# Performance work log

Measured on AMD Instinct MI355X. Metric: run time of the kernel, lower is better.

Reference implementation:

```python
import jax, jax.numpy as jnp
import numpy as np

EMBED_DIM = 1024
NUM_HEADS = 16
HEAD_DIM = EMBED_DIM // NUM_HEADS
VOCAB = 5          # languages
BOTTLENECK = 800
SCALING = HEAD_DIM ** -0.5


def setup_inputs() -> dict:
    key = jax.random.key(0)
    ks = jax.random.split(key, 16)
    T, B, D = 2048, 2, EMBED_DIM
    s = 0.02
    return {
        "query": jax.random.normal(ks[0], (T, B, D), jnp.float32),
        "key": jax.random.normal(ks[1], (T, B, D), jnp.float32),
        "value": jax.random.normal(ks[2], (T, B, D), jnp.float32),
        "wq": jax.random.normal(ks[3], (D, D), jnp.float32) * s,
        "bq": jnp.zeros((D,), jnp.float32),
        "wk": jax.random.normal(ks[4], (D, D), jnp.float32) * s,
        "bk": jnp.zeros((D,), jnp.float32),
        "wv": jax.random.normal(ks[5], (D, D), jnp.float32) * s,
        "bv": jnp.zeros((D,), jnp.float32),
        "wo": jax.random.normal(ks[6], (D, D), jnp.float32) * s,
        "bo": jnp.zeros((D,), jnp.float32),
        "wte": jax.random.normal(ks[7], (VOCAB, D), jnp.float32) * s,
        "ct_w1": jax.random.normal(ks[8], (VOCAB, BOTTLENECK, D), jnp.float32) * s,
        "ct_b1": jnp.zeros((VOCAB, BOTTLENECK), jnp.float32),
        "ct_w2": jax.random.normal(ks[9], (VOCAB, 2 * D, BOTTLENECK), jnp.float32) * s,
        "ct_b2": jnp.zeros((VOCAB, 2 * D), jnp.float32),
        "language_id": jax.random.randint(ks[10], (B,), 0, VOCAB, jnp.int32),
    }


def _prefix_kv(language_id, wte, ct_w1, ct_b1, ct_w2, ct_b2):
    # PrefixTuningLangEmbLangspec: embed lang id, run all 5 bottleneck MLPs,
    # select per-sample MLP output via one-hot weighting, split into K/V.
    B = language_id.shape[0]
    emb = wte[language_id]                                  # [B, D]
    h = jnp.tanh(jnp.einsum("bd,chd->cbh", emb, ct_w1) + ct_b1[:, None, :])  # [5,B,800]
    kv = jnp.einsum("cbh,cdh->cbd", h, ct_w2) + ct_b2[:, None, :]            # [5,B,2D]
    w = jax.nn.one_hot(language_id, VOCAB, dtype=kv.dtype)  # [B,5]
    kv_sel = jnp.einsum("bc,cbd->bd", w, kv)                # [B,2D]
    # view(b,1,2,nh,hd): first D -> keys, second D -> values
    pk = kv_sel[:, :EMBED_DIM].reshape(B, NUM_HEADS, 1, HEAD_DIM)
    pv = kv_sel[:, EMBED_DIM:].reshape(B, NUM_HEADS, 1, HEAD_DIM)
    return pk, pv


def reference(query, key, value, wq, bq, wk, bk, wv, bv, wo, bo,
              wte, ct_w1, ct_b1, ct_w2, ct_b2, language_id):
    T, B, D = query.shape
    pk, pv = _prefix_kv(language_id, wte, ct_w1, ct_b1, ct_w2, ct_b2)  # [B,H,1,hd]

    # separate Q/K/V projections (Linear: x @ W^T + b)
    q = (jnp.einsum("tbd,ed->tbe", query, wq) + bq) * SCALING
    k = jnp.einsum("tbd,ed->tbe", key, wk) + bk
    v = jnp.einsum("tbd,ed->tbe", value, wv) + bv

    # [T,B,D] -> [B,H,T,hd]
    def split_heads(x):
        return x.reshape(T, B, NUM_HEADS, HEAD_DIM).transpose(1, 2, 0, 3)

    qh = split_heads(q)
    kh = jnp.concatenate([pk, split_heads(k)], axis=2)  # [B,H,T+1,hd]
    vh = jnp.concatenate([pv, split_heads(v)], axis=2)

    scores = jnp.einsum("bhqd,bhkd->bhqk", qh, kh)      # [B,H,T,T+1]
    attn = jax.nn.softmax(scores, axis=-1)
    ctx = jnp.einsum("bhqk,bhkd->bhqd", attn, vh)       # [B,H,T,hd]

    ctx = ctx.transpose(2, 0, 1, 3).reshape(T, B, D)    # back to [T,B,D]
    out = jnp.einsum("tbd,ed->tbe", ctx, wo) + bo
    return out
```

## Files before the change

### kernel.cpp

```cpp
#include <hip/hip_runtime.h>
#include <stdint.h>

#define T_SEQ 2048
#define BATCH 2
#define DIM   1024
#define NH    16
#define HD    64
#define TKP   2112

typedef _Float16 v8h __attribute__((ext_vector_type(8)));
typedef _Float16 v4h __attribute__((ext_vector_type(4)));
typedef float    f32x4 __attribute__((ext_vector_type(4)));

__device__ __forceinline__ void gload16(const _Float16* g, _Float16* l) {
  __builtin_amdgcn_global_load_lds(
      (__attribute__((address_space(1))) unsigned int*)g,
      (__attribute__((address_space(3))) unsigned int*)l, 16, 0, 0);
}

__global__ void cvt_all(const float4* __restrict__ s0, const float4* __restrict__ s1,
                        const float4* __restrict__ s2, const float4* __restrict__ s3,
                        const float4* __restrict__ s4, const float4* __restrict__ s5,
                        const float4* __restrict__ s6,
                        v4h* __restrict__ d0, v4h* __restrict__ d1, v4h* __restrict__ d2,
                        v4h* __restrict__ d3, v4h* __restrict__ d4, v4h* __restrict__ d5,
                        v4h* __restrict__ d6) {
  const int NTB4 = 1048576, DD4 = 262144;
  int i = blockIdx.x * 256 + threadIdx.x;
  const float4* s; v4h* d; int off;
  if (i < 3 * NTB4) {
    int t = i / NTB4; off = i - t * NTB4;
    s = t == 0 ? s0 : t == 1 ? s1 : s2;
    d = t == 0 ? d0 : t == 1 ? d1 : d2;
  } else {
    int j = i - 3 * NTB4;
    int t = j / DD4; off = j - t * DD4;
    s = t == 0 ? s3 : t == 1 ? s4 : t == 2 ? s5 : s6;
    d = t == 0 ? d3 : t == 1 ? d4 : t == 2 ? d5 : d6;
  }
  float4 v = s[off];
  v4h o = { (_Float16)v.x, (_Float16)v.y, (_Float16)v.z, (_Float16)v.w };
  d[off] = o;
}

__global__ void prefix_h_k(const float* __restrict__ wte, const float* __restrict__ w1,
                           const float* __restrict__ b1, const int* __restrict__ lang,
                           float* __restrict__ hbuf) {
  int wid = blockIdx.x * 4 + (threadIdx.x >> 6);
  int lane = threadIdx.x & 63;
  int b = wid / 800, j = wid - b * 800;
  int c = lang[b];
  const float* wr = w1 + ((size_t)c * 800 + j) * 1024;
  const float* em = wte + (size_t)c * 1024;
  float s = 0.f;
  for (int d = lane; d < 1024; d += 64) s += wr[d] * em[d];
  for (int off = 32; off > 0; off >>= 1) s += __shfl_down(s, off, 64);
  if (lane == 0) hbuf[wid] = tanhf(s + b1[c * 800 + j]);
}

__global__ void prefix_kv_k(const float* __restrict__ w2, const float* __restrict__ b2,
                            const float* __restrict__ hbuf, const int* __restrict__ lang,
                            _Float16* __restrict__ kb, _Float16* __restrict__ vb) {
  int wid = blockIdx.x * 4 + (threadIdx.x >> 6);
  int lane = threadIdx.x & 63;
  int b = wid >> 11, e = wid & 2047;
  int c = lang[b];
  const float* wr = w2 + ((size_t)c * 2048 + e) * 800;
  const float* hb = hbuf + b * 800;
  float s = 0.f;
  for (int j = lane; j < 800; j += 64) s += wr[j] * hb[j];
  for (int off = 32; off > 0; off >>= 1) s += __shfl_down(s, off, 64);
  if (lane == 0) {
    float val = s + b2[c * 2048 + e];
    if (e < 1024) {
      int h = e >> 6, hd = e & 63;
      kb[((size_t)(b * 16 + h) * TKP + 2048) * 64 + hd] = (_Float16)val;
    } else {
      int d = e - 1024;
      int h = d >> 6, hd = d & 63;
      vb[((size_t)(b * 16 + h) * 64 + hd) * TKP + 2048] = (_Float16)val;
    }
  }
}

__global__ void pad_k(_Float16* kb, _Float16* vb) {
  int bh = blockIdx.x;
  v8h z = {};
  _Float16* kp = kb + ((size_t)bh * TKP + 2048) * 64;
  for (int i = threadIdx.x; i < 512; i += 256) *(v8h*)&kp[i * 8] = z;
  for (int i = threadIdx.x; i < 512; i += 256) {
    int c = i >> 3, seg = i & 7;
    *(v8h*)&vb[((size_t)bh * 64 + c) * TKP + 2048 + seg * 8] = z;
  }
}

__global__ __launch_bounds__(256) void gemm_bt_k(
    const _Float16* __restrict__ A0, const _Float16* __restrict__ A1, const _Float16* __restrict__ A2,
    const _Float16* __restrict__ W0, const _Float16* __restrict__ W1, const _Float16* __restrict__ W2,
    const float* __restrict__ bs0, const float* __restrict__ bs1, const float* __restrict__ bs2,
    _Float16* __restrict__ qb, _Float16* __restrict__ kb, _Float16* __restrict__ vb,
    float* __restrict__ fout, int mode_base)
{
  __shared__ __align__(16) _Float16 smem[128 * 64 * 2];
  _Float16* As = smem;
  _Float16* Bs = smem + 128 * 64;
  const int mode = mode_base + blockIdx.z;
  const _Float16* A = (mode == 1) ? A1 : (mode == 2) ? A2 : A0;
  const _Float16* W = (mode == 1) ? W1 : (mode == 2) ? W2 : W0;
  const float* bias = (mode == 1) ? bs1 : (mode == 2) ? bs2 : bs0;
  const int tid = threadIdx.x, w = tid >> 6, lane = tid & 63;
  const int quad = lane >> 4, l15 = lane & 15;
  const int r0 = blockIdx.x * 128, c0 = blockIdx.y * 128;
  const int wm = w >> 1, wn = w & 1;
  const int srow = lane >> 3, sseg = lane & 7;
  f32x4 acc[4][4] = {};
  for (int k0 = 0; k0 < 1024; k0 += 64) {
    for (int i = 0; i < 4; ++i) {
      int rowb = w * 32 + i * 8;
      gload16(A + (size_t)(r0 + rowb + srow) * 1024 + k0 + sseg * 8, &As[rowb * 64]);
      gload16(W + (size_t)(c0 + rowb + srow) * 1024 + k0 + sseg * 8, &Bs[rowb * 64]);
    }
    __syncthreads();
    for (int ks = 0; ks < 2; ++ks) {
      v8h af[4], bfr[4];
      for (int mt = 0; mt < 4; ++mt)
        af[mt] = *(const v8h*)&As[(wm * 64 + mt * 16 + l15) * 64 + ks * 32 + quad * 8];
      for (int nt = 0; nt < 4; ++nt)
        bfr[nt] = *(const v8h*)&Bs[(wn * 64 + nt * 16 + l15) * 64 + ks * 32 + quad * 8];
      for (int mt = 0; mt < 4; ++mt)
        for (int nt = 0; nt < 4; ++nt)
          acc[mt][nt] = __builtin_amdgcn_mfma_f32_16x16x32_f16(af[mt], bfr[nt], acc[mt][nt], 0, 0, 0);
    }
    __syncthreads();
  }
  if (mode == 3) {
    for (int nt = 0; nt < 4; ++nt) {
      int e = c0 + wn * 64 + nt * 16 + l15;
      float be = bias[e];
      for (int mt = 0; mt < 4; ++mt) {
        int rb = r0 + wm * 64 + mt * 16 + quad * 4;
        for (int reg = 0; reg < 4; ++reg)
          fout[(size_t)(rb + reg) * 1024 + e] = acc[mt][nt][reg] + be;
      }
    }
    return;
  }
  _Float16* st = smem + w * 4096;
  const float qscale = (mode == 0) ? 0.125f : 1.0f;
  for (int p = 0; p < 2; ++p) {
    __syncthreads();
    for (int ntl = 0; ntl < 2; ++ntl) {
      int nt = p * 2 + ntl;
      int e = c0 + wn * 64 + nt * 16 + l15;
      float be = bias[e];
      for (int mt = 0; mt < 4; ++mt)
        for (int reg = 0; reg < 4; ++reg) {
          float val = (acc[mt][nt][reg] + be) * qscale;
          int rl = mt * 16 + quad * 4 + reg;
          if (mode != 2) st[rl * 40 + ntl * 16 + l15] = (_Float16)val;
          else st[(ntl * 16 + l15) * 72 + (rl & 1) * 32 + (rl >> 1)] = (_Float16)val;
        }
    }
    __syncthreads();
    if (mode != 2) {
      for (int it = 0; it < 4; ++it) {
        int chunk = it * 64 + lane;
        int rr = chunk >> 2, seg = chunk & 3;
        v8h val = *(const v8h*)&st[rr * 40 + seg * 8];
        int r = r0 + wm * 64 + rr, b = r & 1, t = r >> 1;
        int e0 = c0 + wn * 64 + p * 32 + seg * 8;
        int h = e0 >> 6, hd0 = e0 & 63;
        if (mode == 0) *(v8h*)&qb[((size_t)(b * 16 + h) * 2048 + t) * 64 + hd0] = val;
        else           *(v8h*)&kb[((size_t)(b * 16 + h) * TKP + t) * 64 + hd0] = val;
      }
    } else {
      for (int it = 0; it < 4; ++it) {
        int chunk = it * 64 + lane;
        int el = chunk >> 3, b = (chunk >> 2) & 1, qs = chunk & 3;
        v8h val = *(const v8h*)&st[el * 72 + b * 32 + qs * 8];
        int e = c0 + wn * 64 + p * 32 + el;
        int h = e >> 6, hd = e & 63;
        int t0 = ((r0 + wm * 64) >> 1) + qs * 8;
        *(v8h*)&vb[((size_t)(b * 16 + h) * 64 + hd) * TKP + t0] = val;
      }
    }
  }
}

__global__ __launch_bounds__(256) void attn_k(
    const _Float16* __restrict__ qb, const _Float16* __restrict__ kb,
    const _Float16* __restrict__ vb, _Float16* __restrict__ ctx)
{
  __shared__ __align__(16) _Float16 Qs[128 * 72];
  __shared__ __align__(16) _Float16 Ks[64 * 72];
  __shared__ __align__(16) _Float16 Vs[64 * 72];
  __shared__ __align__(16) _Float16 Ps[128 * 72];
  const int bh = blockIdx.x;
  const int qt0 = blockIdx.y * 128;
  const int tid = threadIdx.x, w = tid >> 6, lane = tid & 63;
  const int quad = lane >> 4, l15 = lane & 15;
  for (int it = 0; it < 4; ++it) {
    int slot = it * 256 + tid;
    int row = slot >> 3, seg = slot & 7;
    int4 v = *(const int4*)(qb + ((size_t)bh * 2048 + qt0 + row) * 64 + seg * 8);
    *(int4*)&Qs[row * 72 + seg * 8] = v;
  }
  const int sr = tid >> 3, sseg = tid & 7;
  const _Float16* kptr = kb + (size_t)bh * TKP * 64 + sr * 64 + sseg * 8;
  const _Float16* vptr = vb + (size_t)bh * 64 * TKP + (size_t)sr * TKP + sseg * 8;
  int4 kp0 = *(const int4*)kptr, kp1 = *(const int4*)(kptr + 2048);
  int4 vp0 = *(const int4*)vptr, vp1 = *(const int4*)(vptr + 32 * TKP);
  kptr += 4096; vptr += 64;
  f32x4 O[4][2] = {};
  float l_[2] = { 0.f, 0.f };
  for (int kc = 0; kc < 33; ++kc) {
    __syncthreads();
    *(int4*)&Ks[sr * 72 + sseg * 8] = kp0;
    *(int4*)&Ks[(sr + 32) * 72 + sseg * 8] = kp1;
    *(int4*)&Vs[sr * 72 + sseg * 8] = vp0;
    *(int4*)&Vs[(sr + 32) * 72 + sseg * 8] = vp1;
    __syncthreads();
    if (kc < 32) {
      kp0 = *(const int4*)kptr; kp1 = *(const int4*)(kptr + 2048);
      vp0 = *(const int4*)vptr; vp1 = *(const int4*)(vptr + 32 * TKP);
      kptr += 4096; vptr += 64;
    }
    f32x4 S[4][2] = {};
    for (int ks = 0; ks < 2; ++ks) {
      v8h q0 = *(const v8h*)&Qs[(w * 32 + l15) * 72 + ks * 32 + quad * 8];
      v8h q1 = *(const v8h*)&Qs[(w * 32 + 16 + l15) * 72 + ks * 32 + quad * 8];
      for (int mt = 0; mt < 4; ++mt) {
        v8h ak = *(const v8h*)&Ks[(mt * 16 + l15) * 72 + ks * 32 + quad * 8];
        S[mt][0] = __builtin_amdgcn_mfma_f32_16x16x32_f16(ak, q0, S[mt][0], 0, 0, 0);
        S[mt][1] = __builtin_amdgcn_mfma_f32_16x16x32_f16(ak, q1, S[mt][1], 0, 0, 0);
      }
    }
    if (kc == 32) {
      for (int mt = 0; mt < 4; ++mt)
        for (int reg = 0; reg < 4; ++reg)
          if (mt * 16 + quad * 4 + reg > 0) { S[mt][0][reg] = -1e30f; S[mt][1][reg] = -1e30f; }
    }
    for (int nt = 0; nt < 2; ++nt) {
      float rsum = 0.f;
      for (int mt = 0; mt < 4; ++mt) {
        float p0 = __expf(S[mt][nt][0]);
        float p1 = __expf(S[mt][nt][1]);
        float p2 = __expf(S[mt][nt][2]);
        float p3 = __expf(S[mt][nt][3]);
        rsum += (p0 + p1) + (p2 + p3);
        v4h pk4 = { (_Float16)p0, (_Float16)p1, (_Float16)p2, (_Float16)p3 };
        *(v4h*)&Ps[(w * 32 + nt * 16 + l15) * 72 + mt * 16 + quad * 4] = pk4;
      }
      l_[nt] += rsum;
    }
    for (int ks = 0; ks < 2; ++ks) {
      v8h p0 = *(const v8h*)&Ps[(w * 32 + l15) * 72 + ks * 32 + quad * 8];
      v8h p1 = *(const v8h*)&Ps[(w * 32 + 16 + l15) * 72 + ks * 32 + quad * 8];
      for (int ht = 0; ht < 4; ++ht) {
        v8h av = *(const v8h*)&Vs[(ht * 16 + l15) * 72 + ks * 32 + quad * 8];
        O[ht][0] = __builtin_amdgcn_mfma_f32_16x16x32_f16(av, p0, O[ht][0], 0, 0, 0);
        O[ht][1] = __builtin_amdgcn_mfma_f32_16x16x32_f16(av, p1, O[ht][1], 0, 0, 0);
      }
    }
  }
  for (int nt = 0; nt < 2; ++nt) {
    l_[nt] += __shfl_xor(l_[nt], 16, 64);
    l_[nt] += __shfl_xor(l_[nt], 32, 64);
  }
  const int b = bh >> 4, hh = bh & 15;
  for (int nt = 0; nt < 2; ++nt) {
    float inv = 1.f / l_[nt];
    int q = qt0 + w * 32 + nt * 16 + l15;
    for (int ht = 0; ht < 4; ++ht) {
      v4h o4 = { (_Float16)(O[ht][nt][0] * inv), (_Float16)(O[ht][nt][1] * inv),
                 (_Float16)(O[ht][nt][2] * inv), (_Float16)(O[ht][nt][3] * inv) };
      *(v4h*)(ctx + ((size_t)q * 2 + b) * 1024 + hh * 64 + ht * 16 + quad * 4) = o4;
    }
  }
}

extern "C" void kernel_launch(void* const* d_in, const int* in_sizes, int n_in,
                              void* d_out, int out_size, void* d_ws, size_t ws_size,
                              hipStream_t stream) {
  (void)in_sizes; (void)n_in; (void)out_size; (void)ws_size;
  const float* query = (const float*)d_in[0];
  const float* key_  = (const float*)d_in[1];
  const float* value = (const float*)d_in[2];
  const float* wq = (const float*)d_in[3];
  const float* bq = (const float*)d_in[4];
  const float* wk = (const float*)d_in[5];
  const float* bk = (const float*)d_in[6];
  const float* wv = (const float*)d_in[7];
  const float* bv = (const float*)d_in[8];
  const float* wo = (const float*)d_in[9];
  const float* bo = (const float*)d_in[10];
  const float* wte = (const float*)d_in[11];
  const float* w1 = (const float*)d_in[12];
  const float* b1 = (const float*)d_in[13];
  const float* w2 = (const float*)d_in[14];
  const float* b2 = (const float*)d_in[15];
  const int* lang = (const int*)d_in[16];
  float* out = (float*)d_out;

  const size_t NTB = (size_t)T_SEQ * BATCH * DIM;
  const size_t DD  = (size_t)DIM * DIM;
  const size_t KVN = (size_t)BATCH * NH * TKP * HD;
  _Float16* xq  = (_Float16*)d_ws;
  _Float16* xk  = xq + NTB;
  _Float16* xv  = xk + NTB;
  _Float16* wqb = xv + NTB;
  _Float16* wkb = wqb + DD;
  _Float16* wvb = wkb + DD;
  _Float16* wob = wvb + DD;
  _Float16* qbuf = wob + DD;
  _Float16* kbuf = qbuf + NTB;
  _Float16* vbuf = kbuf + KVN;
  float* hbuf = (float*)(vbuf + KVN);
  _Float16* ctxb = xq;

  cvt_all<<<16384, 256, 0, stream>>>((const float4*)query, (const float4*)key_,
                                     (const float4*)value, (const float4*)wq,
                                     (const float4*)wk, (const float4*)wv, (const float4*)wo,
                                     (v4h*)xq, (v4h*)xk, (v4h*)xv, (v4h*)wqb,
                                     (v4h*)wkb, (v4h*)wvb, (v4h*)wob);
  pad_k<<<32, 256, 0, stream>>>(kbuf, vbuf);
  prefix_h_k<<<400, 256, 0, stream>>>(wte, w1, b1, lang, hbuf);
  prefix_kv_k<<<1024, 256, 0, stream>>>(w2, b2, hbuf, lang, kbuf, vbuf);
  gemm_bt_k<<<dim3(32, 8, 3), 256, 0, stream>>>(xq, xk, xv, wqb, wkb, wvb, bq, bk, bv,
                                                qbuf, kbuf, vbuf, nullptr, 0);
  attn_k<<<dim3(32, 16), 256, 0, stream>>>(qbuf, kbuf, vbuf, ctxb);
  gemm_bt_k<<<dim3(32, 8, 1), 256, 0, stream>>>(ctxb, ctxb, ctxb, wob, wob, wob, bo, bo, bo,
                                                qbuf, kbuf, vbuf, out, 3);
}
```

Before: 311.0 us.

## Double-buffer K/V in LDS, keep Q in registers, use exp2 and MFMA row sums

The attention kernel now double-buffers the K/V shared tiles, which removes one barrier per iteration. Q fragments are loaded straight into registers instead of being staged through LDS. The softmax scale is folded with log2(e) into the Q projection so the kernel can use the hardware exp2. Row sums are accumulated by an MFMA against a ones vector rather than scalar adds and cross-lane shuffles. This cuts LDS traffic, barrier cost and VALU work, in exchange for more LDS space for the doubled buffers and extra MFMA issue, with the row sum now taken over fp16-rounded probabilities.

```diff
diff --git a/kernel.cpp b/kernel.cpp
--- a/kernel.cpp
+++ b/kernel.cpp
@@ -146,7 +146,7 @@
     return;
   }
   _Float16* st = smem + w * 4096;
-  const float qscale = (mode == 0) ? 0.125f : 1.0f;
+  const float qscale = (mode == 0) ? 0.125f * 1.44269504088896341f : 1.0f;
   for (int p = 0; p < 2; ++p) {
     __syncthreads();
     for (int ntl = 0; ntl < 2; ++ntl) {
@@ -191,20 +191,18 @@
     const _Float16* __restrict__ qb, const _Float16* __restrict__ kb,
     const _Float16* __restrict__ vb, _Float16* __restrict__ ctx)
 {
-  __shared__ __align__(16) _Float16 Qs[128 * 72];
-  __shared__ __align__(16) _Float16 Ks[64 * 72];
-  __shared__ __align__(16) _Float16 Vs[64 * 72];
+  __shared__ __align__(16) _Float16 Ks[2][64 * 72];
+  __shared__ __align__(16) _Float16 Vs[2][64 * 72];
   __shared__ __align__(16) _Float16 Ps[128 * 72];
   const int bh = blockIdx.x;
   const int qt0 = blockIdx.y * 128;
   const int tid = threadIdx.x, w = tid >> 6, lane = tid & 63;
   const int quad = lane >> 4, l15 = lane & 15;
-  for (int it = 0; it < 4; ++it) {
-    int slot = it * 256 + tid;
-    int row = slot >> 3, seg = slot & 7;
-    int4 v = *(const int4*)(qb + ((size_t)bh * 2048 + qt0 + row) * 64 + seg * 8);
-    *(int4*)&Qs[row * 72 + seg * 8] = v;
-  }
+  v8h qf[2][2];
+  for (int nt = 0; nt < 2; ++nt)
+    for (int ks = 0; ks < 2; ++ks)
+      qf[nt][ks] = *(const v8h*)(qb + ((size_t)bh * 2048 + qt0 + w * 32 + nt * 16 + l15) * 64
+                                 + ks * 32 + quad * 8);
   const int sr = tid >> 3, sseg = tid & 7;
   const _Float16* kptr = kb + (size_t)bh * TKP * 64 + sr * 64 + sseg * 8;
   const _Float16* vptr = vb + (size_t)bh * 64 * TKP + (size_t)sr * TKP + sseg * 8;
@@ -212,13 +210,16 @@
   int4 vp0 = *(const int4*)vptr, vp1 = *(const int4*)(vptr + 32 * TKP);
   kptr += 4096; vptr += 64;
   f32x4 O[4][2] = {};
-  float l_[2] = { 0.f, 0.f };
+  f32x4 lacc[2] = {};
+  const v8h vones = { (_Float16)1.f, (_Float16)1.f, (_Float16)1.f, (_Float16)1.f,
+                      (_Float16)1.f, (_Float16)1.f, (_Float16)1.f, (_Float16)1.f };
   for (int kc = 0; kc < 33; ++kc) {
-    __syncthreads();
-    *(int4*)&Ks[sr * 72 + sseg * 8] = kp0;
-    *(int4*)&Ks[(sr + 32) * 72 + sseg * 8] = kp1;
-    *(int4*)&Vs[sr * 72 + sseg * 8] = vp0;
-    *(int4*)&Vs[(sr + 32) * 72 + sseg * 8] = vp1;
+    _Float16* Kb = Ks[kc & 1];
+    _Float16* Vb = Vs[kc & 1];
+    *(int4*)&Kb[sr * 72 + sseg * 8] = kp0;
+    *(int4*)&Kb[(sr + 32) * 72 + sseg * 8] = kp1;
+    *(int4*)&Vb[sr * 72 + sseg * 8] = vp0;
+    *(int4*)&Vb[(sr + 32) * 72 + sseg * 8] = vp1;
     __syncthreads();
     if (kc < 32) {
       kp0 = *(const int4*)kptr; kp1 = *(const int4*)(kptr + 2048);
@@ -227,12 +228,10 @@
     }
     f32x4 S[4][2] = {};
     for (int ks = 0; ks < 2; ++ks) {
-      v8h q0 = *(const v8h*)&Qs[(w * 32 + l15) * 72 + ks * 32 + quad * 8];
-      v8h q1 = *(const v8h*)&Qs[(w * 32 + 16 + l15) * 72 + ks * 32 + quad * 8];
       for (int mt = 0; mt < 4; ++mt) {
-        v8h ak = *(const v8h*)&Ks[(mt * 16 + l15) * 72 + ks * 32 + quad * 8];
-        S[mt][0] = __builtin_amdgcn_mfma_f32_16x16x32_f16(ak, q0, S[mt][0], 0, 0, 0);
-        S[mt][1] = __builtin_amdgcn_mfma_f32_16x16x32_f16(ak, q1, S[mt][1], 0, 0, 0);
+        v8h ak = *(const v8h*)&Kb[(mt * 16 + l15) * 72 + ks * 32 + quad * 8];
+        S[mt][0] = __builtin_amdgcn_mfma_f32_16x16x32_f16(ak, qf[0][ks], S[mt][0], 0, 0, 0);
+        S[mt][1] = __builtin_amdgcn_mfma_f32_16x16x32_f16(ak, qf[1][ks], S[mt][1], 0, 0, 0);
       }
     }
     if (kc == 32) {
@@ -240,36 +239,29 @@
         for (int reg = 0; reg < 4; ++reg)
           if (mt * 16 + quad * 4 + reg > 0) { S[mt][0][reg] = -1e30f; S[mt][1][reg] = -1e30f; }
     }
-    for (int nt = 0; nt < 2; ++nt) {
-      float rsum = 0.f;
+    for (int nt = 0; nt < 2; ++nt)
       for (int mt = 0; mt < 4; ++mt) {
-        float p0 = __expf(S[mt][nt][0]);
-        float p1 = __expf(S[mt][nt][1]);
-        float p2 = __expf(S[mt][nt][2]);
-        float p3 = __expf(S[mt][nt][3]);
-        rsum += (p0 + p1) + (p2 + p3);
-        v4h pk4 = { (_Float16)p0, (_Float16)p1, (_Float16)p2, (_Float16)p3 };
+        v4h pk4 = { (_Float16)__builtin_amdgcn_exp2f(S[mt][nt][0]),
+                    (_Float16)__builtin_amdgcn_exp2f(S[mt][nt][1]),
+                    (_Float16)__builtin_amdgcn_exp2f(S[mt][nt][2]),
+                    (_Float16)__builtin_amdgcn_exp2f(S[mt][nt][3]) };
         *(v4h*)&Ps[(w * 32 + nt * 16 + l15) * 72 + mt * 16 + quad * 4] = pk4;
       }
-      l_[nt] += rsum;
-    }
     for (int ks = 0; ks < 2; ++ks) {
       v8h p0 = *(const v8h*)&Ps[(w * 32 + l15) * 72 + ks * 32 + quad * 8];
       v8h p1 = *(const v8h*)&Ps[(w * 32 + 16 + l15) * 72 + ks * 32 + quad * 8];
       for (int ht = 0; ht < 4; ++ht) {
-        v8h av = *(const v8h*)&Vs[(ht * 16 + l15) * 72 + ks * 32 + quad * 8];
+        v8h av = *(const v8h*)&Vb[(ht * 16 + l15) * 72 + ks * 32 + quad * 8];
         O[ht][0] = __builtin_amdgcn_mfma_f32_16x16x32_f16(av, p0, O[ht][0], 0, 0, 0);
         O[ht][1] = __builtin_amdgcn_mfma_f32_16x16x32_f16(av, p1, O[ht][1], 0, 0, 0);
       }
-    }
-  }
-  for (int nt = 0; nt < 2; ++nt) {
-    l_[nt] += __shfl_xor(l_[nt], 16, 64);
-    l_[nt] += __shfl_xor(l_[nt], 32, 64);
+      lacc[0] = __builtin_amdgcn_mfma_f32_16x16x32_f16(vones, p0, lacc[0], 0, 0, 0);
+      lacc[1] = __builtin_amdgcn_mfma_f32_16x16x32_f16(vones, p1, lacc[1], 0, 0, 0);
+    }
   }
   const int b = bh >> 4, hh = bh & 15;
   for (int nt = 0; nt < 2; ++nt) {
-    float inv = 1.f / l_[nt];
+    float inv = 1.f / lacc[nt][0];
     int q = qt0 + w * 32 + nt * 16 + l15;
     for (int ht = 0; ht < 4; ++ht) {
       v4h o4 = { (_Float16)(O[ht][nt][0] * inv), (_Float16)(O[ht][nt][1] * inv),
```

Result: no change. 307.5 us (-1.1%).
